# Kernel optimization log

Hardware: AMD Instinct MI355X
Metric: run time of the kernel (lower is better)

Reference implementation:

```python
import jax, jax.numpy as jnp
import numpy as np

D_MODEL = 1024
N_HEADS = 16
D_K = D_MODEL // N_HEADS


def setup_inputs() -> dict:
    key = jax.random.key(0)
    ks = jax.random.split(key, 9)
    s = 1.0 / np.sqrt(D_MODEL)
    x = jax.random.normal(ks[0], (4, 2048, D_MODEL), dtype=jnp.float32)
    def lin(kw, kb):
        W = jax.random.uniform(kw, (D_MODEL, D_MODEL), jnp.float32, -s, s)
        b = jax.random.uniform(kb, (D_MODEL,), jnp.float32, -s, s)
        return W, b
    w_q, b_q = lin(ks[1], ks[2])
    w_k, b_k = lin(ks[3], ks[4])
    w_v, b_v = lin(ks[5], ks[6])
    w_o, b_o = lin(ks[7], ks[8])
    return {"x": x, "w_q": w_q, "b_q": b_q, "w_k": w_k, "b_k": b_k,
            "w_v": w_v, "b_v": b_v, "w_o": w_o, "b_o": b_o}


def reference(x, w_q, b_q, w_k, b_k, w_v, b_v, w_o, b_o):
    B, S, _ = x.shape
    # projections; nn.Linear computes x @ W^T + b, here W stored as [in, out]
    def proj(W, b):
        return (x @ W + b).reshape(B, S, N_HEADS, D_K).transpose(0, 2, 1, 3)  # [B,H,S,Dk]
    q = proj(w_q, b_q)
    k = proj(w_k, b_k)
    v = proj(w_v, b_v)
    scores = jnp.einsum("bhsd,bhtd->bhst", q, k) / jnp.sqrt(jnp.float32(D_K))
    attn = jax.nn.softmax(scores, axis=-1)  # dropout p=0 -> identity
    ctx = jnp.einsum("bhst,bhtd->bhsd", attn, v)
    ctx = ctx.transpose(0, 2, 1, 3).reshape(B, S, D_MODEL)
    return ctx @ w_o + b_o
```

## Files before the change

kernel.cpp:

```cpp
#include <hip/hip_runtime.h>
#include <stdint.h>

typedef __attribute__((ext_vector_type(8))) short bf8;
typedef __attribute__((ext_vector_type(4))) float f4;
typedef __attribute__((ext_vector_type(16))) float f16v;
typedef __attribute__((ext_vector_type(4))) int i4;
typedef __attribute__((ext_vector_type(2))) int i2;
typedef unsigned short u16;

#define GLOAD16(gptr, lptr)                                                        \
    __builtin_amdgcn_global_load_lds((const __attribute__((address_space(1))) void*)(gptr), \
                                     (__attribute__((address_space(3))) void*)(lptr), 16, 0, 0)

static __device__ inline u16 f2bfbits(float f) {
    unsigned u = __float_as_uint(f);
    unsigned r = 0x7FFFu + ((u >> 16) & 1u);
    return (u16)((u + r) >> 16);
}

static __device__ inline int cvtpk(float lo, float hi) {
    int r;
    asm("v_cvt_pk_bf16_f32 %0, %1, %2" : "=v"(r) : "v"(lo), "v"(hi));
    return r;
}

__global__ void cvt_bf16(const float* __restrict__ in, u16* __restrict__ out, int n) {
    int i = (blockIdx.x * 256 + threadIdx.x) * 4;
    if (i < n) {
        float4 v = *(const float4*)(in + i);
        ushort4 o;
        o.x = f2bfbits(v.x); o.y = f2bfbits(v.y);
        o.z = f2bfbits(v.z); o.w = f2bfbits(v.w);
        *(ushort4*)(out + i) = o;
    }
}

__global__ void transpose4(const float* __restrict__ w0, const float* __restrict__ w1,
                           const float* __restrict__ w2, const float* __restrict__ w3,
                           u16* __restrict__ o0, u16* __restrict__ o1,
                           u16* __restrict__ o2, u16* __restrict__ o3) {
    __shared__ float tile[32][33];
    const float* w = blockIdx.z == 0 ? w0 : blockIdx.z == 1 ? w1 : blockIdx.z == 2 ? w2 : w3;
    u16* o = blockIdx.z == 0 ? o0 : blockIdx.z == 1 ? o1 : blockIdx.z == 2 ? o2 : o3;
    int bx = blockIdx.x * 32, by = blockIdx.y * 32;
    int tx = threadIdx.x, ty = threadIdx.y;
#pragma unroll
    for (int r = 0; r < 32; r += 8)
        tile[ty + r][tx] = w[(size_t)(by + ty + r) * 1024 + bx + tx];
    __syncthreads();
#pragma unroll
    for (int r = 0; r < 32; r += 8)
        o[(size_t)(bx + ty + r) * 1024 + by + tx] = f2bfbits(tile[tx][ty + r]);
}

static __device__ __attribute__((always_inline)) void gemm_pipe(
    const u16* __restrict__ A_, const u16* __restrict__ B_, int m0, int n0,
    char* Asl, char* Bsl, f4 (&acc)[4][4]) {
    const int tid = threadIdx.x;
    const int lane = tid & 63;
    const int l15 = lane & 15, lg = lane >> 4;
    const int wave = tid >> 6;
    const int wm = (wave >> 1) * 64, wn = (wave & 1) * 64;
    const int sr = lane >> 2, sc = lane & 3;

    const int rA0 = wave * 32 + sr;
    const int rA1 = rA0 + 16;
    const int cA0 = sc ^ ((rA0 >> 1) & 3);
    const int cA1 = sc ^ ((rA1 >> 1) & 3);
    const u16* pA0 = A_ + (size_t)(m0 + rA0) * 1024 + cA0 * 8;
    const u16* pA1 = A_ + (size_t)(m0 + rA1) * 1024 + cA1 * 8;
    const u16* pB0 = B_ + (size_t)(n0 + rA0) * 1024 + cA0 * 8;
    const u16* pB1 = B_ + (size_t)(n0 + rA1) * 1024 + cA1 * 8;

#pragma unroll
    for (int p = 0; p < 3; ++p) {
        const int k0 = p * 32;
        GLOAD16(pA0 + k0, Asl + p * 8192 + wave * 2048);
        GLOAD16(pA1 + k0, Asl + p * 8192 + wave * 2048 + 1024);
        GLOAD16(pB0 + k0, Bsl + p * 8192 + wave * 2048);
        GLOAD16(pB1 + k0, Bsl + p * 8192 + wave * 2048 + 1024);
    }

    int offA[4], offB[4];
#pragma unroll
    for (int i = 0; i < 4; ++i) {
        int r = wm + i * 16 + l15;
        offA[i] = r * 64 + ((lg ^ ((r >> 1) & 3)) * 16);
    }
#pragma unroll
    for (int j = 0; j < 4; ++j) {
        int r = wn + j * 16 + l15;
        offB[j] = r * 64 + ((lg ^ ((r >> 1) & 3)) * 16);
    }

    int b = 0;
    for (int kt = 0; kt < 32; ++kt) {
        asm volatile("s_waitcnt vmcnt(8)" ::: "memory");
        __builtin_amdgcn_s_barrier();
        __builtin_amdgcn_sched_barrier(0);
        const char* Ab = Asl + b * 8192;
        const char* Bb = Bsl + b * 8192;
        bf8 af[4], bfr[4];
#pragma unroll
        for (int i = 0; i < 4; ++i) af[i] = *(const bf8*)(Ab + offA[i]);
#pragma unroll
        for (int j = 0; j < 4; ++j) bfr[j] = *(const bf8*)(Bb + offB[j]);
        asm volatile("s_waitcnt lgkmcnt(0)" ::: "memory");
        __builtin_amdgcn_sched_barrier(0);
        __builtin_amdgcn_s_setprio(1);
#pragma unroll
        for (int i = 0; i < 4; ++i)
#pragma unroll
            for (int j = 0; j < 4; ++j)
                acc[i][j] = __builtin_amdgcn_mfma_f32_16x16x32_bf16(af[i], bfr[j], acc[i][j], 0, 0, 0);
        __builtin_amdgcn_s_setprio(0);
        __builtin_amdgcn_sched_barrier(0);
        __builtin_amdgcn_s_barrier();
        __builtin_amdgcn_sched_barrier(0);
        {
            const int k0 = ((kt + 3) & 31) * 32;
            GLOAD16(pA0 + k0, Asl + b * 8192 + wave * 2048);
            GLOAD16(pA1 + k0, Asl + b * 8192 + wave * 2048 + 1024);
            GLOAD16(pB0 + k0, Bsl + b * 8192 + wave * 2048);
            GLOAD16(pB1 + k0, Bsl + b * 8192 + wave * 2048 + 1024);
        }
        b = (b == 2) ? 0 : b + 1;
    }
    asm volatile("s_waitcnt vmcnt(0)" ::: "memory");
}

__global__ __launch_bounds__(256, 3) void gemm_qkv(
    const u16* __restrict__ A, const u16* __restrict__ BT,
    const float* __restrict__ bq, const float* __restrict__ bk, const float* __restrict__ bv,
    u16* __restrict__ qo, u16* __restrict__ ko, u16* __restrict__ vo) {
    __shared__ __align__(16) char Asl[24576];
    __shared__ __align__(16) char Bsl[24576];
    const int wg = blockIdx.x;
    const int xcd = wg & 7, idx = wg >> 3;
    const int nt = idx >> 3;
    const int mt = xcd * 8 + (idx & 7);
    const int m0 = mt * 128, n0 = nt * 128;
    f4 acc[4][4] = {};
    gemm_pipe(A, BT, m0, n0, Asl, Bsl, acc);

    const int lane = threadIdx.x & 63;
    const int l15 = lane & 15, lg = lane >> 4;
    const int wave = threadIdx.x >> 6;
    const int wm = (wave >> 1) * 64, wn = (wave & 1) * 64;

    const int reg = n0 >> 10;
    const float* bp = reg == 0 ? bq : reg == 1 ? bk : bv;
    const float scq = reg == 0 ? 0.125f * 1.44269504088896340736f : 1.0f;
    float bj[4];
#pragma unroll
    for (int j = 0; j < 4; ++j) bj[j] = bp[(n0 + wn + j * 16 + l15) & 1023];

    if (reg < 2) {
        u16* outb = reg == 0 ? qo : ko;
#pragma unroll
        for (int i = 0; i < 4; ++i) {
            int gm = m0 + wm + i * 16 + lg * 4;
#pragma unroll
            for (int j = 0; j < 4; ++j) {
                int gn = (n0 + wn + j * 16 + l15) & 1023;
                int h = gn >> 6, d = gn & 63;
#pragma unroll
                for (int r = 0; r < 4; ++r) {
                    int m = gm + r;
                    int b_ = m >> 11, s = m & 2047;
                    float vv = (acc[i][j][r] + bj[j]) * scq;
                    outb[(((size_t)(b_ * 16 + h) * 2048) + s) * 64 + d] = f2bfbits(vv);
                }
            }
        }
    } else {
#pragma unroll
        for (int i = 0; i < 4; ++i) {
            int gm = m0 + wm + i * 16 + lg * 4;
            int b_ = gm >> 11, s0 = gm & 2047;
#pragma unroll
            for (int j = 0; j < 4; ++j) {
                int gn = (n0 + wn + j * 16 + l15) & 1023;
                int h = gn >> 6, d = gn & 63;
                ushort4 w;
                w.x = f2bfbits(acc[i][j][0] + bj[j]);
                w.y = f2bfbits(acc[i][j][1] + bj[j]);
                w.z = f2bfbits(acc[i][j][2] + bj[j]);
                w.w = f2bfbits(acc[i][j][3] + bj[j]);
                *(ushort4*)(vo + ((size_t)(b_ * 16 + h) * 64 + d) * 2048 + s0) = w;
            }
        }
    }
}

__global__ __launch_bounds__(256, 3) void gemm_o(
    const u16* __restrict__ A, const u16* __restrict__ BT,
    const float* __restrict__ bias, float* __restrict__ outf) {
    __shared__ __align__(16) char Asl[24576];
    __shared__ __align__(16) char Bsl[24576];
    const int wg = blockIdx.x;
    const int xcd = wg & 7, idx = wg >> 3;
    const int nt = idx >> 3;
    const int mt = xcd * 8 + (idx & 7);
    const int m0 = mt * 128, n0 = nt * 128;
    f4 acc[4][4] = {};
    gemm_pipe(A, BT, m0, n0, Asl, Bsl, acc);

    const int lane = threadIdx.x & 63;
    const int l15 = lane & 15, lg = lane >> 4;
    const int wave = threadIdx.x >> 6;
    const int wm = (wave >> 1) * 64, wn = (wave & 1) * 64;

    float bj[4];
#pragma unroll
    for (int j = 0; j < 4; ++j) bj[j] = bias[n0 + wn + j * 16 + l15];
#pragma unroll
    for (int i = 0; i < 4; ++i) {
        int gm = m0 + wm + i * 16 + lg * 4;
#pragma unroll
        for (int j = 0; j < 4; ++j) {
            int gn = n0 + wn + j * 16 + l15;
#pragma unroll
            for (int r = 0; r < 4; ++r)
                outf[(size_t)(gm + r) * 1024 + gn] = acc[i][j][r] + bj[j];
        }
    }
}

static __device__ inline void softmax_pv(f16v s, float& l,
                                         f16v& ocA, f16v& ocB, const bf8* vf) {
    float s0 = 0.f, s1 = 0.f, s2 = 0.f, s3 = 0.f;
#pragma unroll
    for (int r = 0; r < 16; r += 4) {
        s[r + 0] = __builtin_amdgcn_exp2f(s[r + 0]); s0 += s[r + 0];
        s[r + 1] = __builtin_amdgcn_exp2f(s[r + 1]); s1 += s[r + 1];
        s[r + 2] = __builtin_amdgcn_exp2f(s[r + 2]); s2 += s[r + 2];
        s[r + 3] = __builtin_amdgcn_exp2f(s[r + 3]); s3 += s[r + 3];
    }
    float ps = (s0 + s1) + (s2 + s3);
    {
        i2 sw = __builtin_amdgcn_permlane32_swap(__float_as_int(ps), __float_as_int(ps), false, false);
        ps = __int_as_float(sw[0]) + __int_as_float(sw[1]);
    }
    l += ps;

    i4 w0, w1;
    {
        i2 r0 = __builtin_amdgcn_permlane32_swap(cvtpk(s[0], s[1]),   cvtpk(s[4], s[5]),   false, false);
        i2 r1 = __builtin_amdgcn_permlane32_swap(cvtpk(s[2], s[3]),   cvtpk(s[6], s[7]),   false, false);
        i2 r2 = __builtin_amdgcn_permlane32_swap(cvtpk(s[8], s[9]),   cvtpk(s[12], s[13]), false, false);
        i2 r3 = __builtin_amdgcn_permlane32_swap(cvtpk(s[10], s[11]), cvtpk(s[14], s[15]), false, false);
        w0[0] = r0[0]; w0[1] = r1[0]; w0[2] = r0[1]; w0[3] = r1[1];
        w1[0] = r2[0]; w1[1] = r3[0]; w1[2] = r2[1]; w1[3] = r3[1];
    }
    union { i4 i; bf8 h; } pa0, pa1;
    pa0.i = w0; pa1.i = w1;

    __builtin_amdgcn_s_setprio(1);
    ocA = __builtin_amdgcn_mfma_f32_32x32x16_bf16(vf[0], pa0.h, ocA, 0, 0, 0);
    ocB = __builtin_amdgcn_mfma_f32_32x32x16_bf16(vf[2], pa0.h, ocB, 0, 0, 0);
    ocA = __builtin_amdgcn_mfma_f32_32x32x16_bf16(vf[1], pa1.h, ocA, 0, 0, 0);
    ocB = __builtin_amdgcn_mfma_f32_32x32x16_bf16(vf[3], pa1.h, ocB, 0, 0, 0);
    __builtin_amdgcn_s_setprio(0);
}

__global__ __launch_bounds__(256, 4) void attn(
    const u16* __restrict__ Q, const u16* __restrict__ K, const u16* __restrict__ VT,
    u16* __restrict__ ctx) {
    __shared__ __align__(16) char Kl[2][8192];
    __shared__ __align__(16) char Vl[2][8192];

    const int tid = threadIdx.x;
    const int lane = tid & 63, wave = tid >> 6;
    const int l31 = lane & 31, hi = lane >> 5;

    const int g = blockIdx.x;
    const int xcd = g & 7, li = g >> 3;
    const int bh = xcd * 8 + (li >> 4);
    const int qblk = li & 15;
    const int q0 = qblk * 128 + wave * 32;

    const char* Kg = (const char*)(K + (size_t)bh * 2048 * 64);
    const char* Vg = (const char*)(VT + (size_t)bh * 64 * 2048);

    const int p0 = wave * 1024 + lane * 16;
    const int p1 = p0 + 4096;
    const int r0 = p0 >> 7, r1 = p1 >> 7;
    const int sc0 = (p0 & 127) ^ ((r0 & 7) << 4);
    const int sc1 = (p1 & 127) ^ ((r1 & 7) << 4);

    bf8 qf[4];
    {
        const u16* Qr = Q + ((size_t)bh * 2048 + q0 + l31) * 64 + hi * 8;
#pragma unroll
        for (int c = 0; c < 4; ++c) qf[c] = *(const bf8*)(Qr + c * 16);
    }

#pragma unroll
    for (int p = 0; p < 2; ++p) {
        GLOAD16(Kg + (size_t)(p * 64 + r0) * 128 + sc0, &Kl[p][wave * 1024]);
        GLOAD16(Kg + (size_t)(p * 64 + r1) * 128 + sc1, &Kl[p][4096 + wave * 1024]);
        GLOAD16(Vg + (size_t)r0 * 4096 + p * 128 + sc0, &Vl[p][wave * 1024]);
        GLOAD16(Vg + (size_t)r1 * 4096 + p * 128 + sc1, &Vl[p][4096 + wave * 1024]);
    }

    f16v oc0 = {}, oc1 = {};
    float l = 0.f;
    const int sw = (l31 & 7) << 4;

    for (int it = 0; it < 32; ++it) {
        const int cur = it & 1;
        asm volatile("s_waitcnt vmcnt(4)" ::: "memory");
        __builtin_amdgcn_s_barrier();
        __builtin_amdgcn_sched_barrier(0);
        const char* Kb = Kl[cur];
        const char* Vb = Vl[cur];

#pragma unroll
        for (int st = 0; st < 2; ++st) {
            bf8 kf[4];
#pragma unroll
            for (int c = 0; c < 4; ++c)
                kf[c] = *(const bf8*)(Kb + (st * 32 + l31) * 128 + ((c * 32 + hi * 16) ^ sw));

            f16v s;
#pragma unroll
            for (int r = 0; r < 16; ++r) s[r] = -10.f;
            __builtin_amdgcn_s_setprio(1);
#pragma unroll
            for (int c = 0; c < 4; ++c)
                s = __builtin_amdgcn_mfma_f32_32x32x16_bf16(kf[c], qf[c], s, 0, 0, 0);
            __builtin_amdgcn_s_setprio(0);

            bf8 vf[4];
#pragma unroll
            for (int dt = 0; dt < 2; ++dt)
#pragma unroll
                for (int tc = 0; tc < 2; ++tc)
                    vf[dt * 2 + tc] = *(const bf8*)(Vb + (dt * 32 + l31) * 128 +
                                                    ((st * 64 + tc * 32 + hi * 16) ^ sw));

            softmax_pv(s, l, oc0, oc1, vf);
        }
        __builtin_amdgcn_sched_barrier(0);
        __builtin_amdgcn_s_barrier();
        __builtin_amdgcn_sched_barrier(0);
        {
            const int tt = (it + 2) & 31;
            GLOAD16(Kg + (size_t)(tt * 64 + r0) * 128 + sc0, &Kl[cur][wave * 1024]);
            GLOAD16(Kg + (size_t)(tt * 64 + r1) * 128 + sc1, &Kl[cur][4096 + wave * 1024]);
            GLOAD16(Vg + (size_t)r0 * 4096 + tt * 128 + sc0, &Vl[cur][wave * 1024]);
            GLOAD16(Vg + (size_t)r1 * 4096 + tt * 128 + sc1, &Vl[cur][4096 + wave * 1024]);
        }
    }

    const int b_ = bh >> 4, hd = bh & 15;
    const float rl = __builtin_amdgcn_rcpf(l);
    u16* Cr = ctx + ((size_t)(b_ * 2048) + q0 + l31) * 1024 + hd * 64;
#pragma unroll
    for (int gi = 0; gi < 4; ++gi) {
        ushort4 w;
        w.x = f2bfbits(oc0[gi * 4 + 0] * rl);
        w.y = f2bfbits(oc0[gi * 4 + 1] * rl);
        w.z = f2bfbits(oc0[gi * 4 + 2] * rl);
        w.w = f2bfbits(oc0[gi * 4 + 3] * rl);
        *(ushort4*)(Cr + gi * 8 + hi * 4) = w;
    }
#pragma unroll
    for (int gi = 0; gi < 4; ++gi) {
        ushort4 w;
        w.x = f2bfbits(oc1[gi * 4 + 0] * rl);
        w.y = f2bfbits(oc1[gi * 4 + 1] * rl);
        w.z = f2bfbits(oc1[gi * 4 + 2] * rl);
        w.w = f2bfbits(oc1[gi * 4 + 3] * rl);
        *(ushort4*)(Cr + 32 + gi * 8 + hi * 4) = w;
    }
}

extern "C" void kernel_launch(void* const* d_in, const int* in_sizes, int n_in,
                              void* d_out, int out_size, void* d_ws, size_t ws_size,
                              hipStream_t stream) {
    const float* x  = (const float*)d_in[0];
    const float* wq = (const float*)d_in[1];
    const float* bq = (const float*)d_in[2];
    const float* wk = (const float*)d_in[3];
    const float* bk = (const float*)d_in[4];
    const float* wv = (const float*)d_in[5];
    const float* bv = (const float*)d_in[6];
    const float* wo = (const float*)d_in[7];
    const float* bo = (const float*)d_in[8];
    float* out = (float*)d_out;

    char* ws = (char*)d_ws;
    u16* xb  = (u16*)ws;
    u16* wtq = (u16*)(ws + (size_t)(16 << 20));
    u16* wtk = wtq + 1024 * 1024;
    u16* wtv = wtk + 1024 * 1024;
    u16* wto = wtv + 1024 * 1024;
    u16* q   = (u16*)(ws + (size_t)(24 << 20));
    u16* k   = q + 8192 * 1024;
    u16* vt  = k + 8192 * 1024;
    u16* ctx = vt + 8192 * 1024;

    hipLaunchKernelGGL(cvt_bf16, dim3(8192), dim3(256), 0, stream, x, xb, 8192 * 1024);
    hipLaunchKernelGGL(transpose4, dim3(32, 32, 4), dim3(32, 8), 0, stream,
                       wq, wk, wv, wo, wtq, wtk, wtv, wto);
    hipLaunchKernelGGL(gemm_qkv, dim3(1536), dim3(256), 0, stream,
                       xb, wtq, bq, bk, bv, q, k, vt);
    hipLaunchKernelGGL(attn, dim3(1024), dim3(256), 0, stream, q, k, vt, ctx);
    hipLaunchKernelGGL(gemm_o, dim3(512), dim3(256), 0, stream, ctx, wto, bo, out);
}
```

Baseline: 189.9 us.

## Rewrite QKV GEMM with 256x128 tiles, 512 threads and BK=64 pipeline

The QKV projection GEMM gets its own main loop with a 256x128 output tile per 512-thread workgroup (8 waves), a K-step of 64 with a new XOR swizzle, and three LDS stages (144 KB) prefetching two steps ahead. Larger tiles halve the grid and raise operand reuse per global load, and each barrier now covers twice the MFMA work. The cost is one workgroup per CU and fewer blocks to hide latency. The epilogue still assumes each wave owns a 64x64 subtile, which matches the new 4x2 wave layout. gemm_o keeps the old shared pipeline.

```diff
diff --git a/kernel.cpp b/kernel.cpp
--- a/kernel.cpp
+++ b/kernel.cpp
@@ -53,100 +53,97 @@
         o[(size_t)(bx + ty + r) * 1024 + by + tx] = f2bfbits(tile[tx][ty + r]);
 }
 
-static __device__ __attribute__((always_inline)) void gemm_pipe(
-    const u16* __restrict__ A_, const u16* __restrict__ B_, int m0, int n0,
-    char* Asl, char* Bsl, f4 (&acc)[4][4]) {
-    const int tid = threadIdx.x;
-    const int lane = tid & 63;
-    const int l15 = lane & 15, lg = lane >> 4;
-    const int wave = tid >> 6;
-    const int wm = (wave >> 1) * 64, wn = (wave & 1) * 64;
-    const int sr = lane >> 2, sc = lane & 3;
-
-    const int rA0 = wave * 32 + sr;
-    const int rA1 = rA0 + 16;
-    const int cA0 = sc ^ ((rA0 >> 1) & 3);
-    const int cA1 = sc ^ ((rA1 >> 1) & 3);
-    const u16* pA0 = A_ + (size_t)(m0 + rA0) * 1024 + cA0 * 8;
-    const u16* pA1 = A_ + (size_t)(m0 + rA1) * 1024 + cA1 * 8;
-    const u16* pB0 = B_ + (size_t)(n0 + rA0) * 1024 + cA0 * 8;
-    const u16* pB1 = B_ + (size_t)(n0 + rA1) * 1024 + cA1 * 8;
-
-#pragma unroll
-    for (int p = 0; p < 3; ++p) {
-        const int k0 = p * 32;
-        GLOAD16(pA0 + k0, Asl + p * 8192 + wave * 2048);
-        GLOAD16(pA1 + k0, Asl + p * 8192 + wave * 2048 + 1024);
-        GLOAD16(pB0 + k0, Bsl + p * 8192 + wave * 2048);
-        GLOAD16(pB1 + k0, Bsl + p * 8192 + wave * 2048 + 1024);
-    }
-
-    int offA[4], offB[4];
-#pragma unroll
-    for (int i = 0; i < 4; ++i) {
-        int r = wm + i * 16 + l15;
-        offA[i] = r * 64 + ((lg ^ ((r >> 1) & 3)) * 16);
-    }
-#pragma unroll
-    for (int j = 0; j < 4; ++j) {
-        int r = wn + j * 16 + l15;
-        offB[j] = r * 64 + ((lg ^ ((r >> 1) & 3)) * 16);
-    }
-
-    int b = 0;
-    for (int kt = 0; kt < 32; ++kt) {
-        asm volatile("s_waitcnt vmcnt(8)" ::: "memory");
-        __builtin_amdgcn_s_barrier();
-        __builtin_amdgcn_sched_barrier(0);
-        const char* Ab = Asl + b * 8192;
-        const char* Bb = Bsl + b * 8192;
-        bf8 af[4], bfr[4];
-#pragma unroll
-        for (int i = 0; i < 4; ++i) af[i] = *(const bf8*)(Ab + offA[i]);
-#pragma unroll
-        for (int j = 0; j < 4; ++j) bfr[j] = *(const bf8*)(Bb + offB[j]);
-        asm volatile("s_waitcnt lgkmcnt(0)" ::: "memory");
-        __builtin_amdgcn_sched_barrier(0);
-        __builtin_amdgcn_s_setprio(1);
-#pragma unroll
-        for (int i = 0; i < 4; ++i)
-#pragma unroll
-            for (int j = 0; j < 4; ++j)
-                acc[i][j] = __builtin_amdgcn_mfma_f32_16x16x32_bf16(af[i], bfr[j], acc[i][j], 0, 0, 0);
-        __builtin_amdgcn_s_setprio(0);
-        __builtin_amdgcn_sched_barrier(0);
-        __builtin_amdgcn_s_barrier();
-        __builtin_amdgcn_sched_barrier(0);
-        {
-            const int k0 = ((kt + 3) & 31) * 32;
-            GLOAD16(pA0 + k0, Asl + b * 8192 + wave * 2048);
-            GLOAD16(pA1 + k0, Asl + b * 8192 + wave * 2048 + 1024);
-            GLOAD16(pB0 + k0, Bsl + b * 8192 + wave * 2048);
-            GLOAD16(pB1 + k0, Bsl + b * 8192 + wave * 2048 + 1024);
-        }
-        b = (b == 2) ? 0 : b + 1;
-    }
-    asm volatile("s_waitcnt vmcnt(0)" ::: "memory");
-}
-
-__global__ __launch_bounds__(256, 3) void gemm_qkv(
+__global__ __launch_bounds__(512, 1) void gemm_qkv(
     const u16* __restrict__ A, const u16* __restrict__ BT,
     const float* __restrict__ bq, const float* __restrict__ bk, const float* __restrict__ bv,
     u16* __restrict__ qo, u16* __restrict__ ko, u16* __restrict__ vo) {
-    __shared__ __align__(16) char Asl[24576];
-    __shared__ __align__(16) char Bsl[24576];
+    __shared__ __align__(16) char Asl[3][32768];
+    __shared__ __align__(16) char Bsl[3][16384];
+
+    const int tid = threadIdx.x;
+    const int lane = tid & 63;
+    const int wid = tid >> 6;
+    const int l15 = lane & 15, lg = lane >> 4;
+    const int wr = wid >> 1, wc = wid & 1;
+    const int wm = wr * 64, wn = wc * 64;
+
     const int wg = blockIdx.x;
     const int xcd = wg & 7, idx = wg >> 3;
-    const int nt = idx >> 3;
-    const int mt = xcd * 8 + (idx & 7);
-    const int m0 = mt * 128, n0 = nt * 128;
+    const int mt = xcd * 4 + (idx & 3);
+    const int nt = idx >> 2;
+    const int m0 = mt * 256, n0 = nt * 128;
+
+    const int srow = wid * 8 + (lane >> 3);
+    const int scolb = ((lane & 7) * 16) ^ ((lane >> 3) << 4);
+    const char* Ag = (const char*)A + ((size_t)(m0 + srow) * 1024) * 2 + scolb;
+    const char* Bg = (const char*)BT + ((size_t)(n0 + srow) * 1024) * 2 + scolb;
+    const int ldso = wid * 1024 + lane * 16;
+
+#pragma unroll
+    for (int p = 0; p < 2; ++p) {
+        const size_t kb = (size_t)p * 128;
+#pragma unroll
+        for (int j = 0; j < 4; ++j)
+            GLOAD16(Ag + (size_t)(j * 64) * 2048 + kb, &Asl[p][j * 8192 + ldso]);
+#pragma unroll
+        for (int j = 0; j < 2; ++j)
+            GLOAD16(Bg + (size_t)(j * 64) * 2048 + kb, &Bsl[p][j * 8192 + ldso]);
+    }
+
+    const int fswz = (l15 & 7) << 4;
+    int offA[4][2], offB[4][2];
+#pragma unroll
+    for (int i = 0; i < 4; ++i)
+#pragma unroll
+        for (int kk = 0; kk < 2; ++kk) {
+            offA[i][kk] = (wm + i * 16 + l15) * 128 + ((kk * 64 + lg * 16) ^ fswz);
+            offB[i][kk] = (wn + i * 16 + l15) * 128 + ((kk * 64 + lg * 16) ^ fswz);
+        }
+
     f4 acc[4][4] = {};
-    gemm_pipe(A, BT, m0, n0, Asl, Bsl, acc);
-
-    const int lane = threadIdx.x & 63;
-    const int l15 = lane & 15, lg = lane >> 4;
-    const int wave = threadIdx.x >> 6;
-    const int wm = (wave >> 1) * 64, wn = (wave & 1) * 64;
+
+    for (int kt = 0; kt < 16; ++kt) {
+        const int b = kt % 3;
+        asm volatile("s_waitcnt vmcnt(6)" ::: "memory");
+        __builtin_amdgcn_s_barrier();
+        __builtin_amdgcn_sched_barrier(0);
+        const char* Ab = Asl[b];
+        const char* Bb = Bsl[b];
+        bf8 af[4][2], bf_[4][2];
+#pragma unroll
+        for (int i = 0; i < 4; ++i)
+#pragma unroll
+            for (int kk = 0; kk < 2; ++kk) {
+                af[i][kk] = *(const bf8*)(Ab + offA[i][kk]);
+                bf_[i][kk] = *(const bf8*)(Bb + offB[i][kk]);
+            }
+        asm volatile("s_waitcnt lgkmcnt(0)" ::: "memory");
+        __builtin_amdgcn_sched_barrier(0);
+        __builtin_amdgcn_s_setprio(1);
+#pragma unroll
+        for (int kk = 0; kk < 2; ++kk)
+#pragma unroll
+            for (int i = 0; i < 4; ++i)
+#pragma unroll
+                for (int j = 0; j < 4; ++j)
+                    acc[i][j] = __builtin_amdgcn_mfma_f32_16x16x32_bf16(af[i][kk], bf_[j][kk], acc[i][j], 0, 0, 0);
+        __builtin_amdgcn_s_setprio(0);
+        __builtin_amdgcn_sched_barrier(0);
+        __builtin_amdgcn_s_barrier();
+        __builtin_amdgcn_sched_barrier(0);
+        {
+            const int ks = (kt + 2) & 15;
+            const int nb = (kt + 2) % 3;
+            const size_t kb = (size_t)ks * 128;
+#pragma unroll
+            for (int j = 0; j < 4; ++j)
+                GLOAD16(Ag + (size_t)(j * 64) * 2048 + kb, &Asl[nb][j * 8192 + ldso]);
+#pragma unroll
+            for (int j = 0; j < 2; ++j)
+                GLOAD16(Bg + (size_t)(j * 64) * 2048 + kb, &Bsl[nb][j * 8192 + ldso]);
+        }
+    }
+    asm volatile("s_waitcnt vmcnt(0)" ::: "memory");
 
     const int reg = n0 >> 10;
     const float* bp = reg == 0 ? bq : reg == 1 ? bk : bv;
@@ -191,6 +188,82 @@
             }
         }
     }
+}
+
+static __device__ __attribute__((always_inline)) void gemm_pipe(
+    const u16* __restrict__ A_, const u16* __restrict__ B_, int m0, int n0,
+    char* Asl, char* Bsl, f4 (&acc)[4][4]) {
+    const int tid = threadIdx.x;
+    const int lane = tid & 63;
+    const int l15 = lane & 15, lg = lane >> 4;
+    const int wave = tid >> 6;
+    const int wm = (wave >> 1) * 64, wn = (wave & 1) * 64;
+    const int sr = lane >> 2, sc = lane & 3;
+
+    const int rA0 = wave * 32 + sr;
+    const int rA1 = rA0 + 16;
+    const int cA0 = sc ^ ((rA0 >> 1) & 3);
+    const int cA1 = sc ^ ((rA1 >> 1) & 3);
+    const u16* pA0 = A_ + (size_t)(m0 + rA0) * 1024 + cA0 * 8;
+    const u16* pA1 = A_ + (size_t)(m0 + rA1) * 1024 + cA1 * 8;
+    const u16* pB0 = B_ + (size_t)(n0 + rA0) * 1024 + cA0 * 8;
+    const u16* pB1 = B_ + (size_t)(n0 + rA1) * 1024 + cA1 * 8;
+
+#pragma unroll
+    for (int p = 0; p < 3; ++p) {
+        const int k0 = p * 32;
+        GLOAD16(pA0 + k0, Asl + p * 8192 + wave * 2048);
+        GLOAD16(pA1 + k0, Asl + p * 8192 + wave * 2048 + 1024);
+        GLOAD16(pB0 + k0, Bsl + p * 8192 + wave * 2048);
+        GLOAD16(pB1 + k0, Bsl + p * 8192 + wave * 2048 + 1024);
+    }
+
+    int offA[4], offB[4];
+#pragma unroll
+    for (int i = 0; i < 4; ++i) {
+        int r = wm + i * 16 + l15;
+        offA[i] = r * 64 + ((lg ^ ((r >> 1) & 3)) * 16);
+    }
+#pragma unroll
+    for (int j = 0; j < 4; ++j) {
+        int r = wn + j * 16 + l15;
+        offB[j] = r * 64 + ((lg ^ ((r >> 1) & 3)) * 16);
+    }
+
+    int b = 0;
+    for (int kt = 0; kt < 32; ++kt) {
+        asm volatile("s_waitcnt vmcnt(8)" ::: "memory");
+        __builtin_amdgcn_s_barrier();
+        __builtin_amdgcn_sched_barrier(0);
+        const char* Ab = Asl + b * 8192;
+        const char* Bb = Bsl + b * 8192;
+        bf8 af[4], bfr[4];
+#pragma unroll
+        for (int i = 0; i < 4; ++i) af[i] = *(const bf8*)(Ab + offA[i]);
+#pragma unroll
+        for (int j = 0; j < 4; ++j) bfr[j] = *(const bf8*)(Bb + offB[j]);
+        asm volatile("s_waitcnt lgkmcnt(0)" ::: "memory");
+        __builtin_amdgcn_sched_barrier(0);
+        __builtin_amdgcn_s_setprio(1);
+#pragma unroll
+        for (int i = 0; i < 4; ++i)
+#pragma unroll
+            for (int j = 0; j < 4; ++j)
+                acc[i][j] = __builtin_amdgcn_mfma_f32_16x16x32_bf16(af[i], bfr[j], acc[i][j], 0, 0, 0);
+        __builtin_amdgcn_s_setprio(0);
+        __builtin_amdgcn_sched_barrier(0);
+        __builtin_amdgcn_s_barrier();
+        __builtin_amdgcn_sched_barrier(0);
+        {
+            const int k0 = ((kt + 3) & 31) * 32;
+            GLOAD16(pA0 + k0, Asl + b * 8192 + wave * 2048);
+            GLOAD16(pA1 + k0, Asl + b * 8192 + wave * 2048 + 1024);
+            GLOAD16(pB0 + k0, Bsl + b * 8192 + wave * 2048);
+            GLOAD16(pB1 + k0, Bsl + b * 8192 + wave * 2048 + 1024);
+        }
+        b = (b == 2) ? 0 : b + 1;
+    }
+    asm volatile("s_waitcnt vmcnt(0)" ::: "memory");
 }
 
 __global__ __launch_bounds__(256, 3) void gemm_o(
@@ -405,7 +478,7 @@
     hipLaunchKernelGGL(cvt_bf16, dim3(8192), dim3(256), 0, stream, x, xb, 8192 * 1024);
     hipLaunchKernelGGL(transpose4, dim3(32, 32, 4), dim3(32, 8), 0, stream,
                        wq, wk, wv, wo, wtq, wtk, wtv, wto);
-    hipLaunchKernelGGL(gemm_qkv, dim3(1536), dim3(256), 0, stream,
+    hipLaunchKernelGGL(gemm_qkv, dim3(768), dim3(512), 0, stream,
                        xb, wtq, bq, bk, bv, q, k, vt);
     hipLaunchKernelGGL(attn, dim3(1024), dim3(256), 0, stream, q, k, vt, ctx);
     hipLaunchKernelGGL(gemm_o, dim3(512), dim3(256), 0, stream, ctx, wto, bo, out);
```

New measurement: 195.9 us. 3.2% more time.
